# Performance work log

Measured on AMD Instinct MI355X. Metric: run time of the kernel, lower is better.

## Reference

```python
import jax, jax.numpy as jnp
import numpy as np
from jax import lax

E = 32          # num_experts
H = 1024        # hidden_size
I = 512         # expert intermediate_size
IS = 2048       # shared expert intermediate_size
G = 8           # n_group
TOPK_GROUP = 4
TOP_K = 8
SCALE = 2.5     # routed_scaling_factor
T = 1024        # tokens


def setup_inputs() -> dict:
    key = jax.random.key(0)
    ks = jax.random.split(key, 9)
    s = 0.02
    return {
        "hidden_states": jax.random.normal(ks[0], (T, H), jnp.float32),
        "gate_w": jax.random.normal(ks[1], (E, H), jnp.float32) * s,
        "e_bias": jax.random.normal(ks[2], (E,), jnp.float32) * 0.1,
        "w_gate": jax.random.normal(ks[3], (E, H, I), jnp.float32) * s,
        "w_up": jax.random.normal(ks[4], (E, H, I), jnp.float32) * s,
        "w_down": jax.random.normal(ks[5], (E, I, H), jnp.float32) * s,
        "ws_gate": jax.random.normal(ks[6], (H, IS), jnp.float32) * s,
        "ws_up": jax.random.normal(ks[7], (H, IS), jnp.float32) * s,
        "ws_down": jax.random.normal(ks[8], (IS, H), jnp.float32) * s,
    }


def _routing_combine(logits, e_bias):
    # Deepseekv3RoutingImpl.noaux_tc (non-fused reference path)
    scores = jax.nn.sigmoid(logits)                    # [T, E]
    swb = scores + e_bias                              # [T, E]
    swb_g = swb.reshape(-1, G, E // G)                 # [T, G, E/G]
    group_scores = lax.top_k(swb_g, 2)[0].sum(-1)      # sum of top-2 per group
    _, gidx = lax.top_k(group_scores, TOPK_GROUP)      # [T, TOPK_GROUP]
    gmask = jax.nn.one_hot(gidx, G, dtype=swb.dtype).sum(1)   # [T, G]
    smask = jnp.repeat(gmask, E // G, axis=-1)         # [T, E]
    _, tidx = lax.top_k(swb * smask, TOP_K)            # [T, TOP_K]
    emask = jax.nn.one_hot(tidx, E, dtype=scores.dtype).sum(1)
    sc = scores * emask
    combine = sc / (sc.sum(-1, keepdims=True) + 1e-20) * SCALE
    return combine, tidx


def reference(hidden_states, gate_w, e_bias, w_gate, w_up, w_down, ws_gate, ws_up, ws_down):
    x = hidden_states
    # gate: fp32 logits
    logits = x.astype(jnp.float32) @ gate_w.T          # [T, E]
    combine, _ = _routing_combine(logits, e_bias)
    # routed experts (FusedMoE math): per-expert gated MLP, combined by routing weights
    h1 = jnp.einsum('th,ehi->tei', x, w_gate)          # [T, E, I]
    h2 = jnp.einsum('th,ehi->tei', x, w_up)
    act = jax.nn.silu(h1) * h2
    routed = jnp.einsum('tei,te,eih->th', act, combine.astype(x.dtype), w_down)
    # shared expert GatedMLP
    shared = (jax.nn.silu(x @ ws_gate) * (x @ ws_up)) @ ws_down
    return routed + shared
```

## Files before the change

### kernel.cpp

```cpp
#include <hip/hip_runtime.h>
#include <cstdint>
#include <cmath>

#define T_TOK 1024
#define H_DIM 1024
#define E_NUM 32
#define I_DIM 512
#define IS_DIM 2048
#define NCOL_R 16384
#define NCOL_T 18432
#define SCALE_F 2.5f
#define MAXTILES 96

typedef __bf16 bf16x8 __attribute__((ext_vector_type(8)));
typedef float f32x4 __attribute__((ext_vector_type(4)));

typedef __attribute__((address_space(3))) unsigned int lds_u32_t;
typedef __attribute__((address_space(1))) const unsigned int glb_u32_t;

__device__ __forceinline__ unsigned short f2b(float f) {
    union { float f; uint32_t u; } v; v.f = f;
    return (unsigned short)((v.u + 0x7FFFu + ((v.u >> 16) & 1u)) >> 16);
}

__device__ __forceinline__ void gll16(const unsigned short* g, unsigned short* l) {
    __builtin_amdgcn_global_load_lds((glb_u32_t*)g, (lds_u32_t*)l, 16, 0, 0);
}

__device__ __forceinline__ void routing_wave(const float* __restrict__ x,
                                             const float* __restrict__ gate_w,
                                             const float* __restrict__ e_bias,
                                             float* __restrict__ combine,
                                             int* __restrict__ topk, int t) {
    int l = threadIdx.x & 63;
    int e = l & 31, half = l >> 5;
    const float4* xr = reinterpret_cast<const float4*>(x + (size_t)t * H_DIM + half * 512);
    const float4* wr = reinterpret_cast<const float4*>(gate_w + (size_t)e * H_DIM + half * 512);
    float s = 0.f;
#pragma unroll 8
    for (int j = 0; j < 128; j++) {
        float4 a = xr[j], b = wr[j];
        s += a.x * b.x + a.y * b.y + a.z * b.z + a.w * b.w;
    }
    s += __shfl_xor(s, 32);
    float sg = 1.f / (1.f + expf(-s));
    float swb = sg + e_bias[e];
    float v1 = __shfl_xor(swb, 1), v2 = __shfl_xor(swb, 2), v3 = __shfl_xor(swb, 3);
    float hi01 = fmaxf(swb, v1), lo01 = fminf(swb, v1);
    float hi23 = fmaxf(v2, v3),  lo23 = fminf(v2, v3);
    float gs = fmaxf(hi01, hi23) + fmaxf(fminf(hi01, hi23), fmaxf(lo01, lo23));
    int g = e >> 2;
    int grank = 0;
#pragma unroll
    for (int gg = 0; gg < 8; gg++) {
        float og = __shfl(gs, gg * 4);
        grank += ((og > gs) || (og == gs && gg < g)) ? 1 : 0;
    }
    bool gsel = grank < 4;
    float candv = gsel ? swb : 0.0f;
    int erank = 0;
#pragma unroll
    for (int ee = 0; ee < 32; ee++) {
        float oc = __shfl(candv, ee);
        erank += ((oc > candv) || (oc == candv && ee < e)) ? 1 : 0;
    }
    bool esel = (erank < 8) && (half == 0);
    unsigned long long m = __ballot(esel);
    int idx = __popcll(m & ((1ull << l) - 1ull));
    if (esel) topk[t * 8 + idx] = e;
    float r = esel ? sg : 0.f;
#pragma unroll
    for (int off = 1; off < 64; off <<= 1) r += __shfl_xor(r, off);
    float inv = SCALE_F / (r + 1e-20f);
    if (half == 0) combine[t * E_NUM + e] = esel ? sg * inv : 0.0f;
}

__global__ __launch_bounds__(256)
void prep_kernel(const float* __restrict__ x, const float* __restrict__ gate_w,
                 const float* __restrict__ e_bias,
                 const float* __restrict__ w_gate, const float* __restrict__ w_up,
                 const float* __restrict__ w_down, const float* __restrict__ ws_gate,
                 const float* __restrict__ ws_up, const float* __restrict__ ws_down,
                 unsigned short* __restrict__ xb, float* __restrict__ combine,
                 int* __restrict__ topk,
                 unsigned short* __restrict__ BG, unsigned short* __restrict__ BU,
                 unsigned short* __restrict__ BDs, unsigned short* __restrict__ SG,
                 unsigned short* __restrict__ SU, unsigned short* __restrict__ BSD) {
    int b = blockIdx.x;
    if (b < 1024) {
        int i = b * 256 + threadIdx.x;
        float4 v = reinterpret_cast<const float4*>(x)[i];
        uint2 o;
        o.x = (uint32_t)f2b(v.x) | ((uint32_t)f2b(v.y) << 16);
        o.y = (uint32_t)f2b(v.z) | ((uint32_t)f2b(v.w) << 16);
        reinterpret_cast<uint2*>(xb)[i] = o;
        return;
    }
    b -= 1024;
    if (b < 256) {
        int t = b * 4 + (threadIdx.x >> 6);
        routing_wave(x, gate_w, e_bias, combine, topk, t);
        return;
    }
    b -= 256;
    const float* src; unsigned short* dst; int C, DS, r0, c0;
    if (b < 4096) {
        int batch = b >> 7, q = b & 127;
        src = w_gate + (size_t)batch * 524288; dst = BG + (size_t)batch * 524288;
        C = 512; DS = 1024; r0 = (q >> 3) * 64; c0 = (q & 7) * 64;
    } else if (b < 8192) {
        b -= 4096; int batch = b >> 7, q = b & 127;
        src = w_up + (size_t)batch * 524288; dst = BU + (size_t)batch * 524288;
        C = 512; DS = 1024; r0 = (q >> 3) * 64; c0 = (q & 7) * 64;
    } else if (b < 12288) {
        b -= 8192; int batch = b >> 7, q = b & 127;
        src = w_down + (size_t)batch * 524288; dst = BDs + (size_t)batch * 524288;
        C = 1024; DS = 512; r0 = (q >> 4) * 64; c0 = (q & 15) * 64;
    } else if (b < 12800) {
        int q = b - 12288;
        src = ws_gate; dst = SG; C = 2048; DS = 1024; r0 = (q >> 5) * 64; c0 = (q & 31) * 64;
    } else if (b < 13312) {
        int q = b - 12800;
        src = ws_up; dst = SU; C = 2048; DS = 1024; r0 = (q >> 5) * 64; c0 = (q & 31) * 64;
    } else {
        int q = b - 13312;
        src = ws_down; dst = BSD; C = 1024; DS = 2048; r0 = (q >> 4) * 64; c0 = (q & 15) * 64;
    }
    __shared__ float tile[64][68];
    int t = threadIdx.x;
    int lr = t >> 4, lc4 = (t & 15) * 4;
#pragma unroll
    for (int p = 0; p < 4; p++) {
        float4 v = *reinterpret_cast<const float4*>(src + (size_t)(r0 + lr + p * 16) * C + c0 + lc4);
        *reinterpret_cast<float4*>(&tile[lr + p * 16][lc4]) = v;
    }
    __syncthreads();
    int oc = t >> 2, orr = (t & 3) * 16;
    uint32_t o[8];
#pragma unroll
    for (int j = 0; j < 8; j++)
        o[j] = (uint32_t)f2b(tile[orr + 2 * j][oc]) | ((uint32_t)f2b(tile[orr + 2 * j + 1][oc]) << 16);
    unsigned short* dp = dst + (size_t)(c0 + oc) * DS + r0 + orr;
    uint4 u0; u0.x = o[0]; u0.y = o[1]; u0.z = o[2]; u0.w = o[3];
    uint4 u1; u1.x = o[4]; u1.y = o[5]; u1.z = o[6]; u1.w = o[7];
    *reinterpret_cast<uint4*>(dp) = u0;
    *reinterpret_cast<uint4*>(dp + 8) = u1;
}

__global__ __launch_bounds__(1024)
void listbuild_kernel(const int* __restrict__ topk, int* __restrict__ meta,
                      int* __restrict__ pair_token, int* __restrict__ slot_of) {
    __shared__ int cnt[E_NUM], start[E_NUM], fill[E_NUM];
    int t = threadIdx.x;
    if (t < E_NUM) cnt[t] = 0;
    __syncthreads();
    int ids[8];
#pragma unroll
    for (int r = 0; r < 8; r++) {
        ids[r] = topk[t * 8 + r];
        atomicAdd(&cnt[ids[r]], 1);
    }
    __syncthreads();
    if (t == 0) {
        int acc = 0;
        for (int e = 0; e < E_NUM; e++) {
            int nt = (cnt[e] + 127) >> 7;
            start[e] = acc * 128;
            fill[e] = 0;
            for (int j = 0; j < nt; j++) meta[1 + acc + j] = e;
            acc += nt;
        }
        meta[0] = acc;
    }
    __syncthreads();
    for (int i = t; i < MAXTILES * 128; i += 1024) pair_token[i] = 0;
    __syncthreads();
#pragma unroll
    for (int r = 0; r < 8; r++) {
        int e = ids[r];
        int s = start[e] + atomicAdd(&fill[e], 1);
        pair_token[s] = t;
        slot_of[t * 8 + r] = s;
    }
}

__global__ __launch_bounds__(256, 2)
void gateup_fused(const unsigned short* __restrict__ xb,
                  const unsigned short* __restrict__ BG,
                  const unsigned short* __restrict__ BU,
                  const unsigned short* __restrict__ SG,
                  const unsigned short* __restrict__ SU,
                  const float* __restrict__ combine,
                  const int* __restrict__ pair_token,
                  const int* __restrict__ meta,
                  unsigned short* __restrict__ act_s,
                  unsigned short* __restrict__ act_sh) {
    int b = blockIdx.x;
    bool routed = b < 384;
    int tid = threadIdx.x, lane = tid & 63, w = tid >> 6;
    int wr = w >> 1, wc = w & 1;
    __shared__ __align__(16) unsigned short lA[2][128 * 32];
    __shared__ __align__(16) unsigned short lBg[2][128 * 32];
    __shared__ __align__(16) unsigned short lBu[2][128 * 32];

    int srow = w * 32 + (lane >> 2);
    int schunk = (lane & 3) * 8;
    int aoff = (w * 32) * 32;

    const unsigned short *gA0, *gA1, *gG0, *gU0;
    int e = 0, slot0 = 0, row0 = 0, ci0 = 0;
    if (routed) {
        int tile = b >> 2;
        if (tile >= meta[0]) return;
        e = meta[1 + tile];
        ci0 = (b & 3) * 128;
        slot0 = tile * 128;
        int brow0 = e * I_DIM + ci0;
        int tok0 = pair_token[slot0 + srow];
        int tok1 = pair_token[slot0 + srow + 16];
        gA0 = xb + (size_t)tok0 * H_DIM + schunk;
        gA1 = xb + (size_t)tok1 * H_DIM + schunk;
        gG0 = BG + (size_t)(brow0 + srow) * H_DIM + schunk;
        gU0 = BU + (size_t)(brow0 + srow) * H_DIM + schunk;
    } else {
        int bb = b - 384;
        row0 = (bb >> 4) * 128;
        ci0 = (bb & 15) * 128;
        gA0 = xb + (size_t)(row0 + srow) * H_DIM + schunk;
        gA1 = gA0 + 16 * H_DIM;
        gG0 = SG + (size_t)(ci0 + srow) * H_DIM + schunk;
        gU0 = SU + (size_t)(ci0 + srow) * H_DIM + schunk;
    }

    f32x4 accg[4][4], accu[4][4];
#pragma unroll
    for (int i = 0; i < 4; i++)
#pragma unroll
        for (int j = 0; j < 4; j++)
#pragma unroll
            for (int r = 0; r < 4; r++) { accg[i][j][r] = 0.f; accu[i][j][r] = 0.f; }

#define GU_STAGE(KK, BSEL)                                        \
    do {                                                          \
        int _k0 = (KK) * 32;                                      \
        unsigned short* _a = &lA[BSEL][aoff];                     \
        gll16(gA0 + _k0, _a);                                     \
        gll16(gA1 + _k0, _a + 16 * 32);                           \
        unsigned short* _g = &lBg[BSEL][aoff];                    \
        gll16(gG0 + _k0, _g);                                     \
        gll16(gG0 + 16 * H_DIM + _k0, _g + 16 * 32);              \
        unsigned short* _u = &lBu[BSEL][aoff];                    \
        gll16(gU0 + _k0, _u);                                     \
        gll16(gU0 + 16 * H_DIM + _k0, _u + 16 * 32);              \
    } while (0)

    GU_STAGE(0, 0);
    __syncthreads();
    for (int kk = 0; kk < 32; kk++) {
        int cur = kk & 1;
        if (kk < 31) GU_STAGE(kk + 1, cur ^ 1);
        bf16x8 af[4], bgf[4], buf2[4];
#pragma unroll
        for (int mi = 0; mi < 4; mi++)
            af[mi] = *reinterpret_cast<const bf16x8*>(
                &lA[cur][(wr * 64 + mi * 16 + (lane & 15)) * 32 + (lane >> 4) * 8]);
#pragma unroll
        for (int ni = 0; ni < 4; ni++) {
            int nn = (wc * 64 + ni * 16 + (lane & 15)) * 32 + (lane >> 4) * 8;
            bgf[ni] = *reinterpret_cast<const bf16x8*>(&lBg[cur][nn]);
            buf2[ni] = *reinterpret_cast<const bf16x8*>(&lBu[cur][nn]);
        }
#pragma unroll
        for (int mi = 0; mi < 4; mi++)
#pragma unroll
            for (int ni = 0; ni < 4; ni++) {
                accg[mi][ni] = __builtin_amdgcn_mfma_f32_16x16x32_bf16(af[mi], bgf[ni], accg[mi][ni], 0, 0, 0);
                accu[mi][ni] = __builtin_amdgcn_mfma_f32_16x16x32_bf16(af[mi], buf2[ni], accu[mi][ni], 0, 0, 0);
            }
        __syncthreads();
    }
#undef GU_STAGE

    int q = lane >> 4, cl = lane & 15;
    if (routed) {
#pragma unroll
        for (int mi = 0; mi < 4; mi++) {
#pragma unroll
            for (int r = 0; r < 4; r++) {
                int row = wr * 64 + mi * 16 + q * 4 + r;
                int token = pair_token[slot0 + row];
                float s = combine[token * E_NUM + e];
#pragma unroll
                for (int ni = 0; ni < 4; ni++) {
                    float g = accg[mi][ni][r], u = accu[mi][ni][r];
                    float a = g / (1.f + expf(-g)) * u * s;
                    act_s[(size_t)(slot0 + row) * I_DIM + ci0 + wc * 64 + ni * 16 + cl] = f2b(a);
                }
            }
        }
    } else {
#pragma unroll
        for (int mi = 0; mi < 4; mi++) {
#pragma unroll
            for (int ni = 0; ni < 4; ni++) {
                int col = ci0 + wc * 64 + ni * 16 + cl;
#pragma unroll
                for (int r = 0; r < 4; r++) {
                    int row = row0 + wr * 64 + mi * 16 + q * 4 + r;
                    float g = accg[mi][ni][r], u = accu[mi][ni][r];
                    float a = g / (1.f + expf(-g)) * u;
                    act_sh[(size_t)row * IS_DIM + col] = f2b(a);
                }
            }
        }
    }
}

__global__ __launch_bounds__(256, 2)
void down_fused(const unsigned short* __restrict__ act_s,
                const unsigned short* __restrict__ BDs,
                const unsigned short* __restrict__ act_sh,
                const unsigned short* __restrict__ BSD,
                const int* __restrict__ meta,
                float* __restrict__ pairpart,
                float* __restrict__ shpart) {
    int b = blockIdx.x;
    bool routed = b < 768;
    int tid = threadIdx.x, lane = tid & 63, w = tid >> 6;
    int wr = w >> 1, wc = w & 1;
    __shared__ __align__(16) unsigned short lA[2][128 * 32];
    __shared__ __align__(16) unsigned short lB[2][128 * 32];

    int srow = w * 32 + (lane >> 2);
    int schunk = (lane & 3) * 8;
    int aoff = (w * 32) * 32;

    const unsigned short *gA0, *gB0;
    size_t ast, bst;
    int kbase, n0, orow;
    float* outp;
    if (routed) {
        int tile = b >> 3;
        if (tile >= meta[0]) return;
        int e = meta[1 + tile];
        n0 = (b & 7) * 128;
        int slot0 = tile * 128;
        gA0 = act_s + (size_t)(slot0 + srow) * I_DIM + schunk;
        gB0 = BDs + (size_t)e * H_DIM * I_DIM + (size_t)(n0 + srow) * I_DIM + schunk;
        ast = I_DIM; bst = I_DIM; kbase = 0;
        outp = pairpart; orow = slot0;
    } else {
        int bb = b - 768;
        int mb = bb >> 5, nb = (bb >> 2) & 7, ks = bb & 3;
        int row0 = mb * 128;
        n0 = nb * 128;
        gA0 = act_sh + (size_t)(row0 + srow) * IS_DIM + schunk;
        gB0 = BSD + (size_t)(n0 + srow) * IS_DIM + schunk;
        ast = IS_DIM; bst = IS_DIM; kbase = ks * 512;
        outp = shpart + ((size_t)ks << 20); orow = row0;
    }

    f32x4 acc[4][4];
#pragma unroll
    for (int i = 0; i < 4; i++)
#pragma unroll
        for (int j = 0; j < 4; j++)
#pragma unroll
            for (int r = 0; r < 4; r++) acc[i][j][r] = 0.f;

#define DN_STAGE(KK, BSEL)                                        \
    do {                                                          \
        size_t _k0 = (size_t)kbase + (size_t)(KK) * 32;           \
        unsigned short* _a = &lA[BSEL][aoff];                     \
        gll16(gA0 + _k0, _a);                                     \
        gll16(gA0 + 16 * ast + _k0, _a + 16 * 32);                \
        unsigned short* _b2 = &lB[BSEL][aoff];                    \
        gll16(gB0 + _k0, _b2);                                    \
        gll16(gB0 + 16 * bst + _k0, _b2 + 16 * 32);               \
    } while (0)

    DN_STAGE(0, 0);
    __syncthreads();
    for (int kk = 0; kk < 16; kk++) {
        int cur = kk & 1;
        if (kk < 15) DN_STAGE(kk + 1, cur ^ 1);
        bf16x8 af[4], bf[4];
#pragma unroll
        for (int mi = 0; mi < 4; mi++)
            af[mi] = *reinterpret_cast<const bf16x8*>(
                &lA[cur][(wr * 64 + mi * 16 + (lane & 15)) * 32 + (lane >> 4) * 8]);
#pragma unroll
        for (int ni = 0; ni < 4; ni++)
            bf[ni] = *reinterpret_cast<const bf16x8*>(
                &lB[cur][(wc * 64 + ni * 16 + (lane & 15)) * 32 + (lane >> 4) * 8]);
#pragma unroll
        for (int mi = 0; mi < 4; mi++)
#pragma unroll
            for (int ni = 0; ni < 4; ni++)
                acc[mi][ni] = __builtin_amdgcn_mfma_f32_16x16x32_bf16(af[mi], bf[ni], acc[mi][ni], 0, 0, 0);
        __syncthreads();
    }
#undef DN_STAGE

    int q = lane >> 4, cl = lane & 15;
#pragma unroll
    for (int mi = 0; mi < 4; mi++) {
#pragma unroll
        for (int ni = 0; ni < 4; ni++) {
            int col = n0 + wc * 64 + ni * 16 + cl;
#pragma unroll
            for (int r = 0; r < 4; r++) {
                int row = orow + wr * 64 + mi * 16 + q * 4 + r;
                outp[(size_t)row * H_DIM + col] = acc[mi][ni][r];
            }
        }
    }
}

__global__ void final_combine(const float* __restrict__ pairpart,
                              const float* __restrict__ shpart,
                              const int* __restrict__ slot_of,
                              float* __restrict__ out) {
    int t = blockIdx.x;
    int h = threadIdx.x * 4;
    float4 o = reinterpret_cast<const float4*>(shpart + (size_t)t * H_DIM + h)[0];
#pragma unroll
    for (int ks = 1; ks < 4; ks++) {
        float4 v = reinterpret_cast<const float4*>(shpart + ((size_t)ks << 20) + (size_t)t * H_DIM + h)[0];
        o.x += v.x; o.y += v.y; o.z += v.z; o.w += v.w;
    }
#pragma unroll
    for (int r = 0; r < 8; r++) {
        int s = slot_of[t * 8 + r];
        float4 v = reinterpret_cast<const float4*>(pairpart + (size_t)s * H_DIM + h)[0];
        o.x += v.x; o.y += v.y; o.z += v.z; o.w += v.w;
    }
    reinterpret_cast<float4*>(out + (size_t)t * H_DIM + h)[0] = o;
}


__global__ void cvt_x_kernel(const float* __restrict__ x, unsigned short* __restrict__ xb) {
    int i = blockIdx.x * 256 + threadIdx.x;
    float4 v = reinterpret_cast<const float4*>(x)[i];
    uint2 o;
    o.x = (uint32_t)f2b(v.x) | ((uint32_t)f2b(v.y) << 16);
    o.y = (uint32_t)f2b(v.z) | ((uint32_t)f2b(v.w) << 16);
    reinterpret_cast<uint2*>(xb)[i] = o;
}

__global__ void routing_kernel(const float* __restrict__ x,
                               const float* __restrict__ gate_w,
                               const float* __restrict__ e_bias,
                               float* __restrict__ combine,
                               int* __restrict__ topk) {
    int t = blockIdx.x;
    routing_wave(x, gate_w, e_bias, combine, topk, t);
}

__global__ __launch_bounds__(256, 2)
void gateup_kernel(const unsigned short* __restrict__ xb,
                   const float* __restrict__ w_gate,
                   const float* __restrict__ w_up,
                   const float* __restrict__ ws_gate,
                   const float* __restrict__ ws_up,
                   const float* __restrict__ combine,
                   unsigned short* __restrict__ act) {
    int mb = blockIdx.x, cb = blockIdx.y;
    int row0 = mb * 128, c0 = cb * 128;
    const float *bg, *bu;
    int bstride, eidx;
    if (c0 < NCOL_R) {
        int e = c0 >> 9, ci = c0 & 511;
        bg = w_gate + (size_t)e * H_DIM * I_DIM + ci;
        bu = w_up   + (size_t)e * H_DIM * I_DIM + ci;
        bstride = I_DIM; eidx = e;
    } else {
        int ci = c0 - NCOL_R;
        bg = ws_gate + ci; bu = ws_up + ci;
        bstride = IS_DIM; eidx = -1;
    }
    __shared__ __align__(16) unsigned short lA[128*32];
    __shared__ __align__(16) unsigned short lBg[128*32];
    __shared__ __align__(16) unsigned short lBu[128*32];
    int tid = threadIdx.x, lane = tid & 63, w = tid >> 6;
    int wr = w >> 1, wc = w & 1;
    f32x4 accg[4][4], accu[4][4];
#pragma unroll
    for (int i = 0; i < 4; i++)
#pragma unroll
        for (int j = 0; j < 4; j++)
#pragma unroll
            for (int r = 0; r < 4; r++) { accg[i][j][r] = 0.f; accu[i][j][r] = 0.f; }
    int ar = tid >> 2, ak = (tid & 3) * 8;
    int bn = tid & 127, bkg = (tid >> 7) * 16;
    for (int kk = 0; kk < H_DIM / 32; kk++) {
        int k0 = kk * 32;
        __syncthreads();
        *reinterpret_cast<uint4*>(&lA[ar*32 + ak]) =
            *reinterpret_cast<const uint4*>(xb + (size_t)(row0 + ar) * H_DIM + k0 + ak);
        *reinterpret_cast<uint4*>(&lA[(ar+64)*32 + ak]) =
            *reinterpret_cast<const uint4*>(xb + (size_t)(row0 + ar + 64) * H_DIM + k0 + ak);
#pragma unroll
        for (int p = 0; p < 4; p++) {
            int kb = bkg + p * 4;
            const float* pg = bg + (size_t)(k0 + kb) * bstride + bn;
            uint2 dg;
            dg.x = (uint32_t)f2b(pg[0])         | ((uint32_t)f2b(pg[bstride])   << 16);
            dg.y = (uint32_t)f2b(pg[2*bstride]) | ((uint32_t)f2b(pg[3*bstride]) << 16);
            *reinterpret_cast<uint2*>(&lBg[bn*32 + kb]) = dg;
            const float* pu = bu + (size_t)(k0 + kb) * bstride + bn;
            uint2 du;
            du.x = (uint32_t)f2b(pu[0])         | ((uint32_t)f2b(pu[bstride])   << 16);
            du.y = (uint32_t)f2b(pu[2*bstride]) | ((uint32_t)f2b(pu[3*bstride]) << 16);
            *reinterpret_cast<uint2*>(&lBu[bn*32 + kb]) = du;
        }
        __syncthreads();
        bf16x8 af[4], bgf[4], buf2[4];
#pragma unroll
        for (int mi = 0; mi < 4; mi++)
            af[mi] = *reinterpret_cast<const bf16x8*>(&lA[(wr*64 + mi*16 + (lane & 15))*32 + (lane >> 4)*8]);
#pragma unroll
        for (int ni = 0; ni < 4; ni++) {
            int nn = (wc*64 + ni*16 + (lane & 15))*32 + (lane >> 4)*8;
            bgf[ni]  = *reinterpret_cast<const bf16x8*>(&lBg[nn]);
            buf2[ni] = *reinterpret_cast<const bf16x8*>(&lBu[nn]);
        }
#pragma unroll
        for (int mi = 0; mi < 4; mi++)
#pragma unroll
            for (int ni = 0; ni < 4; ni++) {
                accg[mi][ni] = __builtin_amdgcn_mfma_f32_16x16x32_bf16(af[mi], bgf[ni],  accg[mi][ni], 0, 0, 0);
                accu[mi][ni] = __builtin_amdgcn_mfma_f32_16x16x32_bf16(af[mi], buf2[ni], accu[mi][ni], 0, 0, 0);
            }
    }
    int q = lane >> 4, cl = lane & 15;
#pragma unroll
    for (int mi = 0; mi < 4; mi++) {
#pragma unroll
        for (int ni = 0; ni < 4; ni++) {
            int colg = c0 + wc*64 + ni*16 + cl;
#pragma unroll
            for (int r = 0; r < 4; r++) {
                int row = row0 + wr*64 + mi*16 + q*4 + r;
                float g = accg[mi][ni][r], u = accu[mi][ni][r];
                float a = g / (1.f + expf(-g)) * u;
                float s = (eidx >= 0) ? combine[row * E_NUM + eidx] : 1.0f;
                act[(size_t)row * NCOL_T + colg] = f2b(a * s);
            }
        }
    }
}

__global__ __launch_bounds__(256, 2)
void down_kernel(const unsigned short* __restrict__ act,
                 const float* __restrict__ w_down,
                 const float* __restrict__ ws_down,
                 float* __restrict__ partials) {
    int mb = blockIdx.x, nb = blockIdx.y, ks = blockIdx.z;
    int row0 = mb * 128, n0 = nb * 128;
    __shared__ __align__(16) unsigned short lA[128*32];
    __shared__ __align__(16) unsigned short lB[128*32];
    int tid = threadIdx.x, lane = tid & 63, w = tid >> 6;
    int wr = w >> 1, wc = w & 1;
    f32x4 acc[4][4];
#pragma unroll
    for (int i = 0; i < 4; i++)
#pragma unroll
        for (int j = 0; j < 4; j++)
#pragma unroll
            for (int r = 0; r < 4; r++) acc[i][j][r] = 0.f;
    int ar = tid >> 2, ak = (tid & 3) * 8;
    int bn = tid & 127, bkg = (tid >> 7) * 16;
    for (int kk = 0; kk < 144; kk++) {
        int k0 = ks * 4608 + kk * 32;
        const float* bb = (k0 < NCOL_R) ? (w_down + (size_t)k0 * H_DIM)
                                        : (ws_down + (size_t)(k0 - NCOL_R) * H_DIM);
        __syncthreads();
        *reinterpret_cast<uint4*>(&lA[ar*32 + ak]) =
            *reinterpret_cast<const uint4*>(act + (size_t)(row0 + ar) * NCOL_T + k0 + ak);
        *reinterpret_cast<uint4*>(&lA[(ar+64)*32 + ak]) =
            *reinterpret_cast<const uint4*>(act + (size_t)(row0 + ar + 64) * NCOL_T + k0 + ak);
#pragma unroll
        for (int p = 0; p < 4; p++) {
            int kb = bkg + p * 4;
            const float* pb = bb + (size_t)kb * H_DIM + n0 + bn;
            uint2 d;
            d.x = (uint32_t)f2b(pb[0])       | ((uint32_t)f2b(pb[H_DIM])   << 16);
            d.y = (uint32_t)f2b(pb[2*H_DIM]) | ((uint32_t)f2b(pb[3*H_DIM]) << 16);
            *reinterpret_cast<uint2*>(&lB[bn*32 + kb]) = d;
        }
        __syncthreads();
        bf16x8 af[4], bf[4];
#pragma unroll
        for (int mi = 0; mi < 4; mi++)
            af[mi] = *reinterpret_cast<const bf16x8*>(&lA[(wr*64 + mi*16 + (lane & 15))*32 + (lane >> 4)*8]);
#pragma unroll
        for (int ni = 0; ni < 4; ni++)
            bf[ni] = *reinterpret_cast<const bf16x8*>(&lB[(wc*64 + ni*16 + (lane & 15))*32 + (lane >> 4)*8]);
#pragma unroll
        for (int mi = 0; mi < 4; mi++)
#pragma unroll
            for (int ni = 0; ni < 4; ni++)
                acc[mi][ni] = __builtin_amdgcn_mfma_f32_16x16x32_bf16(af[mi], bf[ni], acc[mi][ni], 0, 0, 0);
    }
    float* pout = partials + ((size_t)ks << 20);
    int q = lane >> 4, cl = lane & 15;
#pragma unroll
    for (int mi = 0; mi < 4; mi++) {
#pragma unroll
        for (int ni = 0; ni < 4; ni++) {
            int col = n0 + wc*64 + ni*16 + cl;
#pragma unroll
            for (int r = 0; r < 4; r++) {
                int row = row0 + wr*64 + mi*16 + q*4 + r;
                pout[(size_t)row * H_DIM + col] = acc[mi][ni][r];
            }
        }
    }
}

__global__ void reduce_kernel(const float* __restrict__ p, float* __restrict__ out) {
    int i = blockIdx.x * 256 + threadIdx.x;
    float4 a = reinterpret_cast<const float4*>(p)[i];
    float4 b = reinterpret_cast<const float4*>(p + (size_t)1048576)[i];
    float4 c = reinterpret_cast<const float4*>(p + (size_t)2097152)[i];
    float4 d = reinterpret_cast<const float4*>(p + (size_t)3145728)[i];
    float4 o;
    o.x = a.x + b.x + c.x + d.x;
    o.y = a.y + b.y + c.y + d.y;
    o.z = a.z + b.z + c.z + d.z;
    o.w = a.w + b.w + c.w + d.w;
    reinterpret_cast<float4*>(out)[i] = o;
}

extern "C" void kernel_launch(void* const* d_in, const int* in_sizes, int n_in,
                              void* d_out, int out_size, void* d_ws, size_t ws_size,
                              hipStream_t stream) {
    const float* x       = (const float*)d_in[0];
    const float* gate_w  = (const float*)d_in[1];
    const float* e_bias  = (const float*)d_in[2];
    const float* w_gate  = (const float*)d_in[3];
    const float* w_up    = (const float*)d_in[4];
    const float* w_down  = (const float*)d_in[5];
    const float* ws_gate = (const float*)d_in[6];
    const float* ws_up   = (const float*)d_in[7];
    const float* ws_down = (const float*)d_in[8];
    float* out = (float*)d_out;

    char* ws = (char*)d_ws;
    bool fast = ws_size >= 170000384ull;

    if (fast) {
        float* combine      = (float*)(ws);
        int*   topk         = (int*)(ws + 131072);
        int*   meta         = (int*)(ws + 163840);
        int*   pair_token   = (int*)(ws + 164352);
        int*   slot_of      = (int*)(ws + 213504);
        unsigned short* xb  = (unsigned short*)(ws + 262144);
        unsigned short* act_s  = (unsigned short*)(ws + 2359296);
        unsigned short* act_sh = (unsigned short*)(ws + 14942208);
        unsigned short* BG  = (unsigned short*)(ws + 19136512);
        unsigned short* BU  = (unsigned short*)(ws + 52690944);
        unsigned short* SG  = (unsigned short*)(ws + 86245376);
        unsigned short* SU  = (unsigned short*)(ws + 90439680);
        unsigned short* BDs = (unsigned short*)(ws + 94633984);
        unsigned short* BSD = (unsigned short*)(ws + 128188416);
        float* pairpart     = (float*)(ws + 19136512);
        float* shpart       = (float*)(ws + 69468160);

        prep_kernel<<<15104, 256, 0, stream>>>(x, gate_w, e_bias, w_gate, w_up, w_down,
                                               ws_gate, ws_up, ws_down,
                                               xb, combine, topk, BG, BU, BDs, SG, SU, BSD);
        listbuild_kernel<<<1, 1024, 0, stream>>>(topk, meta, pair_token, slot_of);
        gateup_fused<<<512, 256, 0, stream>>>(xb, BG, BU, SG, SU, combine, pair_token, meta,
                                              act_s, act_sh);
        down_fused<<<1024, 256, 0, stream>>>(act_s, BDs, act_sh, BSD, meta, pairpart, shpart);
        final_combine<<<1024, 256, 0, stream>>>(pairpart, shpart, slot_of, out);
    } else {
        float* combine     = (float*)(ws);
        int*   topk        = (int*)(ws + 131072);
        unsigned short* xb = (unsigned short*)(ws + 262144);
        unsigned short* act= (unsigned short*)(ws + 2359296);
        float* partials    = (float*)(ws + 40108032);

        cvt_x_kernel<<<1024, 256, 0, stream>>>(x, xb);
        routing_kernel<<<1024, 64, 0, stream>>>(x, gate_w, e_bias, combine, topk);
        gateup_kernel<<<dim3(8, 144), 256, 0, stream>>>(xb, w_gate, w_up, ws_gate, ws_up, combine, act);
        down_kernel<<<dim3(8, 8, 4), 256, 0, stream>>>(act, w_down, ws_down, partials);
        reduce_kernel<<<1024, 256, 0, stream>>>(partials, out);
    }
}
```

Measured before the change: 343.1 us.

## Move down-weight conversion into gate/up kernel and widen transpose tiles

```diff
diff --git a/kernel.cpp b/kernel.cpp
--- a/kernel.cpp
+++ b/kernel.cpp
@@ -75,17 +75,60 @@
     if (half == 0) combine[t * E_NUM + e] = esel ? sg * inv : 0.0f;
 }
 
+__device__ __forceinline__ void tcvt128_dev(const float* __restrict__ src,
+                                            unsigned short* __restrict__ dst,
+                                            int C, int DS, int r0, int c0,
+                                            float* tbuf) {
+    int t = threadIdx.x;
+    int lr = t >> 4;
+    int c4 = t & 15;
+    float4 v0[4], v1[4];
+    const float* s0 = src + (size_t)(r0 + lr) * C + c0 + c4 * 4;
+#pragma unroll
+    for (int p = 0; p < 4; p++) v0[p] = *reinterpret_cast<const float4*>(s0 + (size_t)p * 16 * C);
+#pragma unroll
+    for (int p = 0; p < 4; p++) v1[p] = *reinterpret_cast<const float4*>(s0 + (size_t)p * 16 * C + 64);
+#pragma unroll
+    for (int p = 0; p < 4; p++) {
+        int row = lr + p * 16;
+        int sc4 = (c4 + (row >> 2) + ((row & 3) << 2)) & 15;
+        *reinterpret_cast<float4*>(&tbuf[row * 64 + sc4 * 4]) = v0[p];
+        *reinterpret_cast<float4*>(&tbuf[4096 + row * 64 + sc4 * 4]) = v1[p];
+    }
+    __syncthreads();
+    int oc = t >> 2, orr = (t & 3) * 16;
+    int ob = oc >> 2, off = oc & 3;
+#pragma unroll
+    for (int half = 0; half < 2; half++) {
+        const float* tb = tbuf + half * 4096;
+        uint32_t o[8];
+#pragma unroll
+        for (int j = 0; j < 8; j++) {
+            int ra = orr + 2 * j, rb = ra + 1;
+            int sa = (ob + (ra >> 2) + ((ra & 3) << 2)) & 15;
+            int sb = (ob + (rb >> 2) + ((rb & 3) << 2)) & 15;
+            float fa = tb[ra * 64 + sa * 4 + off];
+            float fb = tb[rb * 64 + sb * 4 + off];
+            o[j] = (uint32_t)f2b(fa) | ((uint32_t)f2b(fb) << 16);
+        }
+        unsigned short* dp = dst + (size_t)(c0 + half * 64 + oc) * DS + r0 + orr;
+        uint4 u0; u0.x = o[0]; u0.y = o[1]; u0.z = o[2]; u0.w = o[3];
+        uint4 u1; u1.x = o[4]; u1.y = o[5]; u1.z = o[6]; u1.w = o[7];
+        *reinterpret_cast<uint4*>(dp) = u0;
+        *reinterpret_cast<uint4*>(dp + 8) = u1;
+    }
+}
+
 __global__ __launch_bounds__(256)
-void prep_kernel(const float* __restrict__ x, const float* __restrict__ gate_w,
-                 const float* __restrict__ e_bias,
-                 const float* __restrict__ w_gate, const float* __restrict__ w_up,
-                 const float* __restrict__ w_down, const float* __restrict__ ws_gate,
-                 const float* __restrict__ ws_up, const float* __restrict__ ws_down,
-                 unsigned short* __restrict__ xb, float* __restrict__ combine,
-                 int* __restrict__ topk,
-                 unsigned short* __restrict__ BG, unsigned short* __restrict__ BU,
-                 unsigned short* __restrict__ BDs, unsigned short* __restrict__ SG,
-                 unsigned short* __restrict__ SU, unsigned short* __restrict__ BSD) {
+void prep1_kernel(const float* __restrict__ x, const float* __restrict__ gate_w,
+                  const float* __restrict__ e_bias,
+                  const float* __restrict__ w_gate, const float* __restrict__ w_up,
+                  const float* __restrict__ ws_gate, const float* __restrict__ ws_up,
+                  unsigned short* __restrict__ xb, float* __restrict__ combine,
+                  int* __restrict__ topk,
+                  unsigned short* __restrict__ BG, unsigned short* __restrict__ BU,
+                  unsigned short* __restrict__ SG, unsigned short* __restrict__ SU) {
+    __shared__ __align__(16) float tbuf[8192];
     int b = blockIdx.x;
     if (b < 1024) {
         int i = b * 256 + threadIdx.x;
@@ -104,47 +147,22 @@
     }
     b -= 256;
     const float* src; unsigned short* dst; int C, DS, r0, c0;
-    if (b < 4096) {
-        int batch = b >> 7, q = b & 127;
+    if (b < 2048) {
+        int batch = b >> 6, q = b & 63;
         src = w_gate + (size_t)batch * 524288; dst = BG + (size_t)batch * 524288;
-        C = 512; DS = 1024; r0 = (q >> 3) * 64; c0 = (q & 7) * 64;
-    } else if (b < 8192) {
-        b -= 4096; int batch = b >> 7, q = b & 127;
+        C = 512; DS = 1024; r0 = (q >> 2) * 64; c0 = (q & 3) * 128;
+    } else if (b < 4096) {
+        b -= 2048; int batch = b >> 6, q = b & 63;
         src = w_up + (size_t)batch * 524288; dst = BU + (size_t)batch * 524288;
-        C = 512; DS = 1024; r0 = (q >> 3) * 64; c0 = (q & 7) * 64;
-    } else if (b < 12288) {
-        b -= 8192; int batch = b >> 7, q = b & 127;
-        src = w_down + (size_t)batch * 524288; dst = BDs + (size_t)batch * 524288;
-        C = 1024; DS = 512; r0 = (q >> 4) * 64; c0 = (q & 15) * 64;
-    } else if (b < 12800) {
-        int q = b - 12288;
-        src = ws_gate; dst = SG; C = 2048; DS = 1024; r0 = (q >> 5) * 64; c0 = (q & 31) * 64;
-    } else if (b < 13312) {
-        int q = b - 12800;
-        src = ws_up; dst = SU; C = 2048; DS = 1024; r0 = (q >> 5) * 64; c0 = (q & 31) * 64;
+        C = 512; DS = 1024; r0 = (q >> 2) * 64; c0 = (q & 3) * 128;
+    } else if (b < 4352) {
+        int q = b - 4096;
+        src = ws_gate; dst = SG; C = 2048; DS = 1024; r0 = (q >> 4) * 64; c0 = (q & 15) * 128;
     } else {
-        int q = b - 13312;
-        src = ws_down; dst = BSD; C = 1024; DS = 2048; r0 = (q >> 4) * 64; c0 = (q & 15) * 64;
-    }
-    __shared__ float tile[64][68];
-    int t = threadIdx.x;
-    int lr = t >> 4, lc4 = (t & 15) * 4;
-#pragma unroll
-    for (int p = 0; p < 4; p++) {
-        float4 v = *reinterpret_cast<const float4*>(src + (size_t)(r0 + lr + p * 16) * C + c0 + lc4);
-        *reinterpret_cast<float4*>(&tile[lr + p * 16][lc4]) = v;
-    }
-    __syncthreads();
-    int oc = t >> 2, orr = (t & 3) * 16;
-    uint32_t o[8];
-#pragma unroll
-    for (int j = 0; j < 8; j++)
-        o[j] = (uint32_t)f2b(tile[orr + 2 * j][oc]) | ((uint32_t)f2b(tile[orr + 2 * j + 1][oc]) << 16);
-    unsigned short* dp = dst + (size_t)(c0 + oc) * DS + r0 + orr;
-    uint4 u0; u0.x = o[0]; u0.y = o[1]; u0.z = o[2]; u0.w = o[3];
-    uint4 u1; u1.x = o[4]; u1.y = o[5]; u1.z = o[6]; u1.w = o[7];
-    *reinterpret_cast<uint4*>(dp) = u0;
-    *reinterpret_cast<uint4*>(dp + 8) = u1;
+        int q = b - 4352;
+        src = ws_up; dst = SU; C = 2048; DS = 1024; r0 = (q >> 4) * 64; c0 = (q & 15) * 128;
+    }
+    tcvt128_dev(src, dst, C, DS, r0, c0, tbuf);
 }
 
 __global__ __launch_bounds__(1024)
@@ -193,15 +211,35 @@
                   const float* __restrict__ combine,
                   const int* __restrict__ pair_token,
                   const int* __restrict__ meta,
+                  const float* __restrict__ w_down,
+                  const float* __restrict__ ws_down,
+                  unsigned short* __restrict__ BDs,
+                  unsigned short* __restrict__ BSD,
                   unsigned short* __restrict__ act_s,
                   unsigned short* __restrict__ act_sh) {
+    __shared__ __align__(16) unsigned short smem[24576];
     int b = blockIdx.x;
+    if (b >= 512) {
+        float* tbuf = reinterpret_cast<float*>(smem);
+        int bb = b - 512;
+        const float* src; unsigned short* dst; int C, DS, r0, c0;
+        if (bb < 2048) {
+            int batch = bb >> 6, q = bb & 63;
+            src = w_down + (size_t)batch * 524288; dst = BDs + (size_t)batch * 524288;
+            C = 1024; DS = 512; r0 = (q >> 3) * 64; c0 = (q & 7) * 128;
+        } else {
+            int q = bb - 2048;
+            src = ws_down; dst = BSD; C = 1024; DS = 2048; r0 = (q >> 3) * 64; c0 = (q & 7) * 128;
+        }
+        tcvt128_dev(src, dst, C, DS, r0, c0, tbuf);
+        return;
+    }
     bool routed = b < 384;
     int tid = threadIdx.x, lane = tid & 63, w = tid >> 6;
     int wr = w >> 1, wc = w & 1;
-    __shared__ __align__(16) unsigned short lA[2][128 * 32];
-    __shared__ __align__(16) unsigned short lBg[2][128 * 32];
-    __shared__ __align__(16) unsigned short lBu[2][128 * 32];
+    unsigned short* lA  = smem;
+    unsigned short* lBg = smem + 8192;
+    unsigned short* lBu = smem + 16384;
 
     int srow = w * 32 + (lane >> 2);
     int schunk = (lane & 3) * 8;
@@ -243,13 +281,13 @@
 #define GU_STAGE(KK, BSEL)                                        \
     do {                                                          \
         int _k0 = (KK) * 32;                                      \
-        unsigned short* _a = &lA[BSEL][aoff];                     \
+        unsigned short* _a = lA + (BSEL) * 4096 + aoff;           \
         gll16(gA0 + _k0, _a);                                     \
         gll16(gA1 + _k0, _a + 16 * 32);                           \
-        unsigned short* _g = &lBg[BSEL][aoff];                    \
+        unsigned short* _g = lBg + (BSEL) * 4096 + aoff;          \
         gll16(gG0 + _k0, _g);                                     \
         gll16(gG0 + 16 * H_DIM + _k0, _g + 16 * 32);              \
-        unsigned short* _u = &lBu[BSEL][aoff];                    \
+        unsigned short* _u = lBu + (BSEL) * 4096 + aoff;          \
         gll16(gU0 + _k0, _u);                                     \
         gll16(gU0 + 16 * H_DIM + _k0, _u + 16 * 32);              \
     } while (0)
@@ -263,12 +301,12 @@
 #pragma unroll
         for (int mi = 0; mi < 4; mi++)
             af[mi] = *reinterpret_cast<const bf16x8*>(
-                &lA[cur][(wr * 64 + mi * 16 + (lane & 15)) * 32 + (lane >> 4) * 8]);
+                &lA[cur * 4096 + (wr * 64 + mi * 16 + (lane & 15)) * 32 + (lane >> 4) * 8]);
 #pragma unroll
         for (int ni = 0; ni < 4; ni++) {
-            int nn = (wc * 64 + ni * 16 + (lane & 15)) * 32 + (lane >> 4) * 8;
-            bgf[ni] = *reinterpret_cast<const bf16x8*>(&lBg[cur][nn]);
-            buf2[ni] = *reinterpret_cast<const bf16x8*>(&lBu[cur][nn]);
+            int nn = cur * 4096 + (wc * 64 + ni * 16 + (lane & 15)) * 32 + (lane >> 4) * 8;
+            bgf[ni] = *reinterpret_cast<const bf16x8*>(&lBg[nn]);
+            buf2[ni] = *reinterpret_cast<const bf16x8*>(&lBu[nn]);
         }
 #pragma unroll
         for (int mi = 0; mi < 4; mi++)
@@ -668,12 +706,12 @@
         float* pairpart     = (float*)(ws + 19136512);
         float* shpart       = (float*)(ws + 69468160);
 
-        prep_kernel<<<15104, 256, 0, stream>>>(x, gate_w, e_bias, w_gate, w_up, w_down,
-                                               ws_gate, ws_up, ws_down,
-                                               xb, combine, topk, BG, BU, BDs, SG, SU, BSD);
+        prep1_kernel<<<5888, 256, 0, stream>>>(x, gate_w, e_bias, w_gate, w_up,
+                                               ws_gate, ws_up,
+                                               xb, combine, topk, BG, BU, SG, SU);
         listbuild_kernel<<<1, 1024, 0, stream>>>(topk, meta, pair_token, slot_of);
-        gateup_fused<<<512, 256, 0, stream>>>(xb, BG, BU, SG, SU, combine, pair_token, meta,
-                                              act_s, act_sh);
+        gateup_fused<<<2816, 256, 0, stream>>>(xb, BG, BU, SG, SU, combine, pair_token, meta,
+                                               w_down, ws_down, BDs, BSD, act_s, act_sh);
         down_fused<<<1024, 256, 0, stream>>>(act_s, BDs, act_sh, BSD, meta, pairpart, shpart);
         final_combine<<<1024, 256, 0, stream>>>(pairpart, shpart, slot_of, out);
     } else {
```

New measurement: 338.7 us. About the same (-1.3%).

## Convert fp32 weights to bf16 inside GEMM loaders instead of separate transpose pass

Applied to the files above, without the earlier changes.

```diff
diff --git a/kernel.cpp b/kernel.cpp
--- a/kernel.cpp
+++ b/kernel.cpp
@@ -21,6 +21,12 @@
 __device__ __forceinline__ unsigned short f2b(float f) {
     union { float f; uint32_t u; } v; v.f = f;
     return (unsigned short)((v.u + 0x7FFFu + ((v.u >> 16) & 1u)) >> 16);
+}
+
+__device__ __forceinline__ uint32_t cvt2(float lo, float hi) {
+    uint32_t r;
+    asm("v_cvt_pk_bf16_f32 %0, %1, %2" : "=v"(r) : "v"(lo), "v"(hi));
+    return r;
 }
 
 __device__ __forceinline__ void gll16(const unsigned short* g, unsigned short* l) {
@@ -76,75 +82,26 @@
 }
 
 __global__ __launch_bounds__(256)
-void prep_kernel(const float* __restrict__ x, const float* __restrict__ gate_w,
-                 const float* __restrict__ e_bias,
-                 const float* __restrict__ w_gate, const float* __restrict__ w_up,
-                 const float* __restrict__ w_down, const float* __restrict__ ws_gate,
-                 const float* __restrict__ ws_up, const float* __restrict__ ws_down,
-                 unsigned short* __restrict__ xb, float* __restrict__ combine,
-                 int* __restrict__ topk,
-                 unsigned short* __restrict__ BG, unsigned short* __restrict__ BU,
-                 unsigned short* __restrict__ BDs, unsigned short* __restrict__ SG,
-                 unsigned short* __restrict__ SU, unsigned short* __restrict__ BSD) {
+void prep1_kernel(const float* __restrict__ x, const float* __restrict__ gate_w,
+                  const float* __restrict__ e_bias,
+                  unsigned short* __restrict__ xb, float* __restrict__ combine,
+                  int* __restrict__ topk) {
     int b = blockIdx.x;
-    if (b < 1024) {
-        int i = b * 256 + threadIdx.x;
-        float4 v = reinterpret_cast<const float4*>(x)[i];
-        uint2 o;
-        o.x = (uint32_t)f2b(v.x) | ((uint32_t)f2b(v.y) << 16);
-        o.y = (uint32_t)f2b(v.z) | ((uint32_t)f2b(v.w) << 16);
-        reinterpret_cast<uint2*>(xb)[i] = o;
-        return;
-    }
-    b -= 1024;
     if (b < 256) {
         int t = b * 4 + (threadIdx.x >> 6);
         routing_wave(x, gate_w, e_bias, combine, topk, t);
         return;
     }
-    b -= 256;
-    const float* src; unsigned short* dst; int C, DS, r0, c0;
-    if (b < 4096) {
-        int batch = b >> 7, q = b & 127;
-        src = w_gate + (size_t)batch * 524288; dst = BG + (size_t)batch * 524288;
-        C = 512; DS = 1024; r0 = (q >> 3) * 64; c0 = (q & 7) * 64;
-    } else if (b < 8192) {
-        b -= 4096; int batch = b >> 7, q = b & 127;
-        src = w_up + (size_t)batch * 524288; dst = BU + (size_t)batch * 524288;
-        C = 512; DS = 1024; r0 = (q >> 3) * 64; c0 = (q & 7) * 64;
-    } else if (b < 12288) {
-        b -= 8192; int batch = b >> 7, q = b & 127;
-        src = w_down + (size_t)batch * 524288; dst = BDs + (size_t)batch * 524288;
-        C = 1024; DS = 512; r0 = (q >> 4) * 64; c0 = (q & 15) * 64;
-    } else if (b < 12800) {
-        int q = b - 12288;
-        src = ws_gate; dst = SG; C = 2048; DS = 1024; r0 = (q >> 5) * 64; c0 = (q & 31) * 64;
-    } else if (b < 13312) {
-        int q = b - 12800;
-        src = ws_up; dst = SU; C = 2048; DS = 1024; r0 = (q >> 5) * 64; c0 = (q & 31) * 64;
-    } else {
-        int q = b - 13312;
-        src = ws_down; dst = BSD; C = 1024; DS = 2048; r0 = (q >> 4) * 64; c0 = (q & 15) * 64;
-    }
-    __shared__ float tile[64][68];
-    int t = threadIdx.x;
-    int lr = t >> 4, lc4 = (t & 15) * 4;
+    int bb = b - 256;
 #pragma unroll
     for (int p = 0; p < 4; p++) {
-        float4 v = *reinterpret_cast<const float4*>(src + (size_t)(r0 + lr + p * 16) * C + c0 + lc4);
-        *reinterpret_cast<float4*>(&tile[lr + p * 16][lc4]) = v;
-    }
-    __syncthreads();
-    int oc = t >> 2, orr = (t & 3) * 16;
-    uint32_t o[8];
-#pragma unroll
-    for (int j = 0; j < 8; j++)
-        o[j] = (uint32_t)f2b(tile[orr + 2 * j][oc]) | ((uint32_t)f2b(tile[orr + 2 * j + 1][oc]) << 16);
-    unsigned short* dp = dst + (size_t)(c0 + oc) * DS + r0 + orr;
-    uint4 u0; u0.x = o[0]; u0.y = o[1]; u0.z = o[2]; u0.w = o[3];
-    uint4 u1; u1.x = o[4]; u1.y = o[5]; u1.z = o[6]; u1.w = o[7];
-    *reinterpret_cast<uint4*>(dp) = u0;
-    *reinterpret_cast<uint4*>(dp + 8) = u1;
+        int i = bb * 1024 + p * 256 + threadIdx.x;
+        float4 v = reinterpret_cast<const float4*>(x)[i];
+        uint2 o;
+        o.x = cvt2(v.x, v.y);
+        o.y = cvt2(v.z, v.w);
+        reinterpret_cast<uint2*>(xb)[i] = o;
+    }
 }
 
 __global__ __launch_bounds__(1024)
@@ -186,10 +143,10 @@
 
 __global__ __launch_bounds__(256, 2)
 void gateup_fused(const unsigned short* __restrict__ xb,
-                  const unsigned short* __restrict__ BG,
-                  const unsigned short* __restrict__ BU,
-                  const unsigned short* __restrict__ SG,
-                  const unsigned short* __restrict__ SU,
+                  const float* __restrict__ w_gate,
+                  const float* __restrict__ w_up,
+                  const float* __restrict__ ws_gate,
+                  const float* __restrict__ ws_up,
                   const float* __restrict__ combine,
                   const int* __restrict__ pair_token,
                   const int* __restrict__ meta,
@@ -200,14 +157,16 @@
     int tid = threadIdx.x, lane = tid & 63, w = tid >> 6;
     int wr = w >> 1, wc = w & 1;
     __shared__ __align__(16) unsigned short lA[2][128 * 32];
-    __shared__ __align__(16) unsigned short lBg[2][128 * 32];
-    __shared__ __align__(16) unsigned short lBu[2][128 * 32];
+    __shared__ __align__(16) unsigned short lBg[2][128 * 40];
+    __shared__ __align__(16) unsigned short lBu[2][128 * 40];
 
     int srow = w * 32 + (lane >> 2);
     int schunk = (lane & 3) * 8;
     int aoff = (w * 32) * 32;
 
-    const unsigned short *gA0, *gA1, *gG0, *gU0;
+    const unsigned short *gA0, *gA1;
+    const float *gBg, *gBu;
+    int bstride;
     int e = 0, slot0 = 0, row0 = 0, ci0 = 0;
     if (routed) {
         int tile = b >> 2;
@@ -215,22 +174,24 @@
         e = meta[1 + tile];
         ci0 = (b & 3) * 128;
         slot0 = tile * 128;
-        int brow0 = e * I_DIM + ci0;
         int tok0 = pair_token[slot0 + srow];
         int tok1 = pair_token[slot0 + srow + 16];
         gA0 = xb + (size_t)tok0 * H_DIM + schunk;
         gA1 = xb + (size_t)tok1 * H_DIM + schunk;
-        gG0 = BG + (size_t)(brow0 + srow) * H_DIM + schunk;
-        gU0 = BU + (size_t)(brow0 + srow) * H_DIM + schunk;
+        gBg = w_gate + (size_t)e * H_DIM * I_DIM + ci0;
+        gBu = w_up   + (size_t)e * H_DIM * I_DIM + ci0;
+        bstride = I_DIM;
     } else {
         int bb = b - 384;
         row0 = (bb >> 4) * 128;
         ci0 = (bb & 15) * 128;
         gA0 = xb + (size_t)(row0 + srow) * H_DIM + schunk;
         gA1 = gA0 + 16 * H_DIM;
-        gG0 = SG + (size_t)(ci0 + srow) * H_DIM + schunk;
-        gU0 = SU + (size_t)(ci0 + srow) * H_DIM + schunk;
-    }
+        gBg = ws_gate + ci0;
+        gBu = ws_up + ci0;
+        bstride = IS_DIM;
+    }
+    int bcol = tid & 127, khalf = tid >> 7;
 
     f32x4 accg[4][4], accu[4][4];
 #pragma unroll
@@ -240,25 +201,53 @@
 #pragma unroll
             for (int r = 0; r < 4; r++) { accg[i][j][r] = 0.f; accu[i][j][r] = 0.f; }
 
-#define GU_STAGE(KK, BSEL)                                        \
-    do {                                                          \
-        int _k0 = (KK) * 32;                                      \
-        unsigned short* _a = &lA[BSEL][aoff];                     \
-        gll16(gA0 + _k0, _a);                                     \
-        gll16(gA1 + _k0, _a + 16 * 32);                           \
-        unsigned short* _g = &lBg[BSEL][aoff];                    \
-        gll16(gG0 + _k0, _g);                                     \
-        gll16(gG0 + 16 * H_DIM + _k0, _g + 16 * 32);              \
-        unsigned short* _u = &lBu[BSEL][aoff];                    \
-        gll16(gU0 + _k0, _u);                                     \
-        gll16(gU0 + 16 * H_DIM + _k0, _u + 16 * 32);              \
+    float rg[16], ru[16];
+
+#define GU_LOADB(KK)                                                    \
+    do {                                                                \
+        size_t kb = (size_t)((KK) * 32 + khalf * 16);                   \
+        _Pragma("unroll")                                               \
+        for (int j = 0; j < 16; j++) {                                  \
+            rg[j] = gBg[(kb + j) * bstride + bcol];                     \
+            ru[j] = gBu[(kb + j) * bstride + bcol];                     \
+        }                                                               \
     } while (0)
 
-    GU_STAGE(0, 0);
+#define GU_GLLA(KK, BSEL)                                               \
+    do {                                                                \
+        int _k0 = (KK) * 32;                                            \
+        unsigned short* _a = &lA[BSEL][aoff];                           \
+        gll16(gA0 + _k0, _a);                                           \
+        gll16(gA1 + _k0, _a + 16 * 32);                                 \
+    } while (0)
+
+#define GU_WRB(BSEL)                                                    \
+    do {                                                                \
+        uint4 u;                                                        \
+        unsigned short* dg = &lBg[BSEL][bcol * 40 + khalf * 16];        \
+        u.x = cvt2(rg[0], rg[1]);  u.y = cvt2(rg[2], rg[3]);            \
+        u.z = cvt2(rg[4], rg[5]);  u.w = cvt2(rg[6], rg[7]);            \
+        *reinterpret_cast<uint4*>(dg) = u;                              \
+        u.x = cvt2(rg[8], rg[9]);  u.y = cvt2(rg[10], rg[11]);          \
+        u.z = cvt2(rg[12], rg[13]); u.w = cvt2(rg[14], rg[15]);         \
+        *reinterpret_cast<uint4*>(dg + 8) = u;                          \
+        unsigned short* du = &lBu[BSEL][bcol * 40 + khalf * 16];        \
+        u.x = cvt2(ru[0], ru[1]);  u.y = cvt2(ru[2], ru[3]);            \
+        u.z = cvt2(ru[4], ru[5]);  u.w = cvt2(ru[6], ru[7]);            \
+        *reinterpret_cast<uint4*>(du) = u;                              \
+        u.x = cvt2(ru[8], ru[9]);  u.y = cvt2(ru[10], ru[11]);          \
+        u.z = cvt2(ru[12], ru[13]); u.w = cvt2(ru[14], ru[15]);         \
+        *reinterpret_cast<uint4*>(du + 8) = u;                          \
+    } while (0)
+
+    GU_GLLA(0, 0);
+    GU_LOADB(0);
+    __syncthreads();
+    GU_WRB(0);
     __syncthreads();
     for (int kk = 0; kk < 32; kk++) {
         int cur = kk & 1;
-        if (kk < 31) GU_STAGE(kk + 1, cur ^ 1);
+        if (kk < 31) { GU_GLLA(kk + 1, cur ^ 1); GU_LOADB(kk + 1); }
         bf16x8 af[4], bgf[4], buf2[4];
 #pragma unroll
         for (int mi = 0; mi < 4; mi++)
@@ -266,7 +255,7 @@
                 &lA[cur][(wr * 64 + mi * 16 + (lane & 15)) * 32 + (lane >> 4) * 8]);
 #pragma unroll
         for (int ni = 0; ni < 4; ni++) {
-            int nn = (wc * 64 + ni * 16 + (lane & 15)) * 32 + (lane >> 4) * 8;
+            int nn = (wc * 64 + ni * 16 + (lane & 15)) * 40 + (lane >> 4) * 8;
             bgf[ni] = *reinterpret_cast<const bf16x8*>(&lBg[cur][nn]);
             buf2[ni] = *reinterpret_cast<const bf16x8*>(&lBu[cur][nn]);
         }
@@ -278,8 +267,14 @@
                 accu[mi][ni] = __builtin_amdgcn_mfma_f32_16x16x32_bf16(af[mi], buf2[ni], accu[mi][ni], 0, 0, 0);
             }
         __syncthreads();
-    }
-#undef GU_STAGE
+        if (kk < 31) {
+            GU_WRB(cur ^ 1);
+            __syncthreads();
+        }
+    }
+#undef GU_LOADB
+#undef GU_GLLA
+#undef GU_WRB
 
     int q = lane >> 4, cl = lane & 15;
     if (routed) {
@@ -316,11 +311,11 @@
     }
 }
 
-__global__ __launch_bounds__(256, 2)
+__global__ __launch_bounds__(256, 3)
 void down_fused(const unsigned short* __restrict__ act_s,
-                const unsigned short* __restrict__ BDs,
+                const float* __restrict__ w_down,
                 const unsigned short* __restrict__ act_sh,
-                const unsigned short* __restrict__ BSD,
+                const float* __restrict__ ws_down,
                 const int* __restrict__ meta,
                 float* __restrict__ pairpart,
                 float* __restrict__ shpart) {
@@ -329,14 +324,15 @@
     int tid = threadIdx.x, lane = tid & 63, w = tid >> 6;
     int wr = w >> 1, wc = w & 1;
     __shared__ __align__(16) unsigned short lA[2][128 * 32];
-    __shared__ __align__(16) unsigned short lB[2][128 * 32];
+    __shared__ __align__(16) unsigned short lB[2][128 * 40];
 
     int srow = w * 32 + (lane >> 2);
     int schunk = (lane & 3) * 8;
     int aoff = (w * 32) * 32;
 
-    const unsigned short *gA0, *gB0;
-    size_t ast, bst;
+    const unsigned short* gA0;
+    const float* gB;
+    size_t ast;
     int kbase, n0, orow;
     float* outp;
     if (routed) {
@@ -346,8 +342,8 @@
         n0 = (b & 7) * 128;
         int slot0 = tile * 128;
         gA0 = act_s + (size_t)(slot0 + srow) * I_DIM + schunk;
-        gB0 = BDs + (size_t)e * H_DIM * I_DIM + (size_t)(n0 + srow) * I_DIM + schunk;
-        ast = I_DIM; bst = I_DIM; kbase = 0;
+        gB = w_down + (size_t)e * I_DIM * H_DIM + n0;
+        ast = I_DIM; kbase = 0;
         outp = pairpart; orow = slot0;
     } else {
         int bb = b - 768;
@@ -355,10 +351,11 @@
         int row0 = mb * 128;
         n0 = nb * 128;
         gA0 = act_sh + (size_t)(row0 + srow) * IS_DIM + schunk;
-        gB0 = BSD + (size_t)(n0 + srow) * IS_DIM + schunk;
-        ast = IS_DIM; bst = IS_DIM; kbase = ks * 512;
+        gB = ws_down + n0;
+        ast = IS_DIM; kbase = ks * 512;
         outp = shpart + ((size_t)ks << 20); orow = row0;
     }
+    int bcol = tid & 127, khalf = tid >> 7;
 
     f32x4 acc[4][4];
 #pragma unroll
@@ -368,22 +365,44 @@
 #pragma unroll
             for (int r = 0; r < 4; r++) acc[i][j][r] = 0.f;
 
-#define DN_STAGE(KK, BSEL)                                        \
-    do {                                                          \
-        size_t _k0 = (size_t)kbase + (size_t)(KK) * 32;           \
-        unsigned short* _a = &lA[BSEL][aoff];                     \
-        gll16(gA0 + _k0, _a);                                     \
-        gll16(gA0 + 16 * ast + _k0, _a + 16 * 32);                \
-        unsigned short* _b2 = &lB[BSEL][aoff];                    \
-        gll16(gB0 + _k0, _b2);                                    \
-        gll16(gB0 + 16 * bst + _k0, _b2 + 16 * 32);               \
+    float rb[16];
+
+#define DN_LOADB(KK)                                                    \
+    do {                                                                \
+        size_t kb = (size_t)(kbase + (KK) * 32 + khalf * 16);           \
+        _Pragma("unroll")                                               \
+        for (int j = 0; j < 16; j++)                                    \
+            rb[j] = gB[(kb + j) * H_DIM + bcol];                        \
     } while (0)
 
-    DN_STAGE(0, 0);
+#define DN_GLLA(KK, BSEL)                                               \
+    do {                                                                \
+        size_t _k0 = (size_t)kbase + (size_t)(KK) * 32;                 \
+        unsigned short* _a = &lA[BSEL][aoff];                           \
+        gll16(gA0 + _k0, _a);                                           \
+        gll16(gA0 + 16 * ast + _k0, _a + 16 * 32);                      \
+    } while (0)
+
+#define DN_WRB(BSEL)                                                    \
+    do {                                                                \
+        uint4 u;                                                        \
+        unsigned short* d = &lB[BSEL][bcol * 40 + khalf * 16];          \
+        u.x = cvt2(rb[0], rb[1]);  u.y = cvt2(rb[2], rb[3]);            \
+        u.z = cvt2(rb[4], rb[5]);  u.w = cvt2(rb[6], rb[7]);            \
+        *reinterpret_cast<uint4*>(d) = u;                               \
+        u.x = cvt2(rb[8], rb[9]);  u.y = cvt2(rb[10], rb[11]);          \
+        u.z = cvt2(rb[12], rb[13]); u.w = cvt2(rb[14], rb[15]);         \
+        *reinterpret_cast<uint4*>(d + 8) = u;                           \
+    } while (0)
+
+    DN_GLLA(0, 0);
+    DN_LOADB(0);
+    __syncthreads();
+    DN_WRB(0);
     __syncthreads();
     for (int kk = 0; kk < 16; kk++) {
         int cur = kk & 1;
-        if (kk < 15) DN_STAGE(kk + 1, cur ^ 1);
+        if (kk < 15) { DN_GLLA(kk + 1, cur ^ 1); DN_LOADB(kk + 1); }
         bf16x8 af[4], bf[4];
 #pragma unroll
         for (int mi = 0; mi < 4; mi++)
@@ -392,15 +411,21 @@
 #pragma unroll
         for (int ni = 0; ni < 4; ni++)
             bf[ni] = *reinterpret_cast<const bf16x8*>(
-                &lB[cur][(wc * 64 + ni * 16 + (lane & 15)) * 32 + (lane >> 4) * 8]);
+                &lB[cur][(wc * 64 + ni * 16 + (lane & 15)) * 40 + (lane >> 4) * 8]);
 #pragma unroll
         for (int mi = 0; mi < 4; mi++)
 #pragma unroll
             for (int ni = 0; ni < 4; ni++)
                 acc[mi][ni] = __builtin_amdgcn_mfma_f32_16x16x32_bf16(af[mi], bf[ni], acc[mi][ni], 0, 0, 0);
         __syncthreads();
-    }
-#undef DN_STAGE
+        if (kk < 15) {
+            DN_WRB(cur ^ 1);
+            __syncthreads();
+        }
+    }
+#undef DN_LOADB
+#undef DN_GLLA
+#undef DN_WRB
 
     int q = lane >> 4, cl = lane & 15;
 #pragma unroll
@@ -659,22 +684,15 @@
         unsigned short* xb  = (unsigned short*)(ws + 262144);
         unsigned short* act_s  = (unsigned short*)(ws + 2359296);
         unsigned short* act_sh = (unsigned short*)(ws + 14942208);
-        unsigned short* BG  = (unsigned short*)(ws + 19136512);
-        unsigned short* BU  = (unsigned short*)(ws + 52690944);
-        unsigned short* SG  = (unsigned short*)(ws + 86245376);
-        unsigned short* SU  = (unsigned short*)(ws + 90439680);
-        unsigned short* BDs = (unsigned short*)(ws + 94633984);
-        unsigned short* BSD = (unsigned short*)(ws + 128188416);
         float* pairpart     = (float*)(ws + 19136512);
         float* shpart       = (float*)(ws + 69468160);
 
-        prep_kernel<<<15104, 256, 0, stream>>>(x, gate_w, e_bias, w_gate, w_up, w_down,
-                                               ws_gate, ws_up, ws_down,
-                                               xb, combine, topk, BG, BU, BDs, SG, SU, BSD);
+        prep1_kernel<<<512, 256, 0, stream>>>(x, gate_w, e_bias, xb, combine, topk);
         listbuild_kernel<<<1, 1024, 0, stream>>>(topk, meta, pair_token, slot_of);
-        gateup_fused<<<512, 256, 0, stream>>>(xb, BG, BU, SG, SU, combine, pair_token, meta,
-                                              act_s, act_sh);
-        down_fused<<<1024, 256, 0, stream>>>(act_s, BDs, act_sh, BSD, meta, pairpart, shpart);
+        gateup_fused<<<512, 256, 0, stream>>>(xb, w_gate, w_up, ws_gate, ws_up,
+                                              combine, pair_token, meta, act_s, act_sh);
+        down_fused<<<1024, 256, 0, stream>>>(act_s, w_down, act_sh, ws_down, meta,
+                                             pairpart, shpart);
         final_combine<<<1024, 256, 0, stream>>>(pairpart, shpart, slot_of, out);
     } else {
         float* combine     = (float*)(ws);
```

Result: no change. 337.8 us (-1.6%).
